# Kernel optimization log

Measured on AMD Instinct MI355X. Metric: run time of the kernel, lower is better.

## Reference

```python
import jax, jax.numpy as jnp
import numpy as np

N_EMBD = 512
N_HEADS = 8
HEAD_DIM = N_EMBD // N_HEADS
LN_EPS = 1e-5


def _layernorm(x):
    # elementwise_affine=False LayerNorm over last dim
    mu = jnp.mean(x, axis=-1, keepdims=True)
    var = jnp.mean(jnp.square(x - mu), axis=-1, keepdims=True)
    return (x - mu) * jax.lax.rsqrt(var + LN_EPS)


def setup_inputs() -> dict:
    key = jax.random.key(0)
    ks = jax.random.split(key, 9)
    B, T, C = 4, 2048, N_EMBD
    s = 0.02
    return {
        "x": jax.random.normal(ks[0], (B, T, C), jnp.float32),
        # SelfAttention: bias arg receives 0.2 (truthy) -> kqv & projection have bias
        "w_kqv": jax.random.normal(ks[1], (3 * C, C), jnp.float32) * s,
        "b_kqv": jax.random.normal(ks[2], (3 * C,), jnp.float32) * s,
        "w_proj": jax.random.normal(ks[3], (C, C), jnp.float32) * s,
        "b_proj": jax.random.normal(ks[4], (C,), jnp.float32) * s,
        # MLP: c_fc has bias=True, c_proj has bias=False
        "w_fc": jax.random.normal(ks[5], (2 * C, C), jnp.float32) * s,
        "b_fc": jax.random.normal(ks[6], (2 * C,), jnp.float32) * s,
        "w_cproj": jax.random.normal(ks[7], (C, 2 * C), jnp.float32) * s,
    }


def _attention(x, w_kqv, b_kqv, w_proj, b_proj):
    B, T, C = x.shape
    kqv = x @ w_kqv.T + b_kqv                      # (B,T,3C)
    kqv = kqv.reshape(B, T, 3, N_HEADS, HEAD_DIM)
    kqv = jnp.transpose(kqv, (2, 0, 3, 1, 4))      # (3,B,H,T,d)
    k, q, v = kqv[0], kqv[1], kqv[2]               # note: k first, as in source
    scores = jnp.einsum("bhqd,bhkd->bhqk", q, k) * (HEAD_DIM ** -0.5)
    attn = jax.nn.softmax(scores, axis=-1)         # dropout = identity (eval)
    agg = jnp.einsum("bhqk,bhkd->bhqd", attn, v)   # (B,H,T,d)
    agg = jnp.transpose(agg, (0, 2, 1, 3)).reshape(B, T, C)
    return agg @ w_proj.T + b_proj


def _mlp(x, w_fc, b_fc, w_cproj):
    h = jax.nn.gelu(x @ w_fc.T + b_fc, approximate=False)  # exact GELU (nn.GELU default)
    return h @ w_cproj.T                                   # c_proj bias=False


def reference(x, w_kqv, b_kqv, w_proj, b_proj, w_fc, b_fc, w_cproj):
    x = x + _attention(_layernorm(x), w_kqv, b_kqv, w_proj, b_proj)
    x = x + _mlp(_layernorm(x), w_fc, b_fc, w_cproj)
    return x
```

## Files before the change

kernel.cpp:

```cpp
#include <hip/hip_runtime.h>
#include <hip/hip_bf16.h>
#include <cmath>


using u16 = unsigned short;
typedef __attribute__((ext_vector_type(4))) float f32x4;
typedef __attribute__((ext_vector_type(16))) float f32x16;
typedef __attribute__((ext_vector_type(8))) short bf16x8;

constexpr int B_ = 4, T_ = 2048, C_ = 512, H_ = 8, D_ = 64;
constexpr int BT = B_ * T_;
constexpr int KQV_SEC = B_ * H_ * T_ * D_;

__device__ __forceinline__ float b2f(u16 u) {
    return __uint_as_float(((unsigned)u) << 16);
}
__device__ __forceinline__ u16 f2b(float f) {
    __hip_bfloat16 h = __float2bfloat16(f);
    return *reinterpret_cast<u16*>(&h);
}
__device__ __forceinline__ float fexp2(float x) {
    float r;
    asm("v_exp_f32 %0, %1" : "=v"(r) : "v"(x));
    return r;
}
__device__ __forceinline__ float frcp(float x) {
    float r;
    asm("v_rcp_f32 %0, %1" : "=v"(r) : "v"(x));
    return r;
}
__device__ __forceinline__ float gelu_f(float v) {
    const float ax = fabsf(v) * 0.70710678118654752f;
    const float t = frcp(1.0f + 0.3275911f * ax);
    const float y = t * (0.254829592f + t * (-0.284496736f + t * (1.421413741f +
                    t * (-1.453152027f + t * 1.061405429f))));
    const float e = fexp2(-ax * ax * 1.44269504088896f);
    float erfv = 1.0f - y * e;
    erfv = copysignf(erfv, v);
    return 0.5f * v * (1.0f + erfv);
}

__device__ __forceinline__ void gl_lds16(const u16* g, u16* l) {
    __builtin_amdgcn_global_load_lds(
        (const __attribute__((address_space(1))) unsigned int*)(const void*)g,
        (__attribute__((address_space(3))) unsigned int*)(void*)l, 16, 0, 0);
}

__device__ __forceinline__ void ln_row(const float* __restrict__ x,
                                       u16* __restrict__ o, int r, int lane) {
    const float4 a = *(const float4*)(x + (size_t)r * C_ + lane * 4);
    const float4 b = *(const float4*)(x + (size_t)r * C_ + 256 + lane * 4);
    float s = (a.x + a.y) + (a.z + a.w) + (b.x + b.y) + (b.z + b.w);
    float q = (a.x * a.x + a.y * a.y) + (a.z * a.z + a.w * a.w) +
              (b.x * b.x + b.y * b.y) + (b.z * b.z + b.w * b.w);
#pragma unroll
    for (int off = 1; off < 64; off <<= 1) {
        s += __shfl_xor(s, off, 64);
        q += __shfl_xor(q, off, 64);
    }
    const float m = s * (1.0f / C_);
    const float var = q * (1.0f / C_) - m * m;
    const float rstd = rsqrtf(var + 1e-5f);
    ushort4 u0, u1;
    u0.x = f2b((a.x - m) * rstd); u0.y = f2b((a.y - m) * rstd);
    u0.z = f2b((a.z - m) * rstd); u0.w = f2b((a.w - m) * rstd);
    u1.x = f2b((b.x - m) * rstd); u1.y = f2b((b.y - m) * rstd);
    u1.z = f2b((b.z - m) * rstd); u1.w = f2b((b.w - m) * rstd);
    *(ushort4*)(o + (size_t)r * C_ + lane * 4) = u0;
    *(ushort4*)(o + (size_t)r * C_ + 256 + lane * 4) = u1;
}

__global__ __launch_bounds__(256) void prep_k(const float* __restrict__ x,
                                              u16* __restrict__ lnout,
                                              const float* __restrict__ w0,
                                              const float* __restrict__ w1,
                                              const float* __restrict__ w2,
                                              const float* __restrict__ w3,
                                              u16* __restrict__ o0,
                                              u16* __restrict__ o1,
                                              u16* __restrict__ o2,
                                              u16* __restrict__ o3) {
    const int bid = blockIdx.x;
    const int t = threadIdx.x;
    if (bid < BT / 4) {
        ln_row(x, lnout, bid * 4 + (t >> 6), t & 63);
    } else {
        const int i = (bid - BT / 4) * 256 + t;
        const float* w; u16* o; int j;
        if (i < 196608) { w = w0; o = o0; j = i; }
        else if (i < 262144) { w = w1; o = o1; j = i - 196608; }
        else if (i < 393216) { w = w2; o = o2; j = i - 262144; }
        else { w = w3; o = o3; j = i - 393216; }
        float4 v = ((const float4*)w)[j];
        ushort4 u;
        u.x = f2b(v.x); u.y = f2b(v.y); u.z = f2b(v.z); u.w = f2b(v.w);
        ((ushort4*)o)[j] = u;
    }
}

__global__ __launch_bounds__(256) void ln_wave_k(const float* __restrict__ x,
                                                 u16* __restrict__ o) {
    ln_row(x, o, blockIdx.x * 4 + (threadIdx.x >> 6), threadIdx.x & 63);
}

template <int EPI, int MT>
__global__ __launch_bounds__(512) void gemm_mfma(const u16* __restrict__ A,
                                                 const u16* __restrict__ W,
                                                 const float* __restrict__ bias,
                                                 const float* __restrict__ resid,
                                                 void* __restrict__ out,
                                                 int K, int N) {
    __shared__ alignas(16) u16 Al[2][MT * 64];
    __shared__ alignas(16) u16 Bl[2][128 * 64];
    const int tid = threadIdx.x, lane = tid & 63, w = tid >> 6;
    const int g = lane >> 4, c = lane & 15;
    const int wm = w >> 1, wn = w & 1;
    const int n0 = blockIdx.x * 128, r0 = blockIdx.y * MT;

    const int l7 = lane & 7, l3 = lane >> 3;
    const int colHalf = ((l7 ^ l3) << 3);

    constexpr int MF = MT / 64;
    f32x4 acc[MF][4] = {};

    auto stage = [&](int buf, int kk) {
        if constexpr (MT == 128) {
#pragma unroll
            for (int i = 0; i < 2; ++i) {
                const int s = w * 2 + i;
                const int row = s * 8 + l3;
                gl_lds16(A + (size_t)(r0 + row) * K + kk + colHalf, &Al[buf][s * 512]);
            }
        } else {
            const int s = w;
            const int row = s * 8 + l3;
            gl_lds16(A + (size_t)(r0 + row) * K + kk + colHalf, &Al[buf][s * 512]);
        }
#pragma unroll
        for (int i = 0; i < 2; ++i) {
            const int s = w * 2 + i;
            const int row = s * 8 + l3;
            gl_lds16(W + (size_t)(n0 + row) * K + kk + colHalf, &Bl[buf][s * 512]);
        }
    };

    stage(0, 0);
    __syncthreads();
    const int NK = K >> 6;
    for (int k8 = 0; k8 < NK; ++k8) {
        const int buf = k8 & 1;
        if (k8 + 1 < NK) stage(buf ^ 1, (k8 + 1) * 64);
        const char* AlB = (const char*)Al[buf];
        const char* BlB = (const char*)Bl[buf];

        bf16x8 af[MF][2], bf[4][2];
#pragma unroll
        for (int mf = 0; mf < MF; ++mf) {
            const int ar = wm * (MT / 4) + mf * 16 + c;
#pragma unroll
            for (int ch = 0; ch < 2; ++ch)
                af[mf][ch] = *(const bf16x8*)(
                    AlB + ar * 128 + (((ch * 32 + g * 8) * 2) ^ ((ar & 7) << 4)));
        }
#pragma unroll
        for (int nf = 0; nf < 4; ++nf) {
            const int br = wn * 64 + nf * 16 + c;
#pragma unroll
            for (int ch = 0; ch < 2; ++ch)
                bf[nf][ch] = *(const bf16x8*)(
                    BlB + br * 128 + (((ch * 32 + g * 8) * 2) ^ ((br & 7) << 4)));
        }
#pragma unroll
        for (int mf = 0; mf < MF; ++mf)
#pragma unroll
            for (int nf = 0; nf < 4; ++nf)
#pragma unroll
                for (int ch = 0; ch < 2; ++ch)
                    acc[mf][nf] = __builtin_amdgcn_mfma_f32_16x16x32_bf16(
                        af[mf][ch], bf[nf][ch], acc[mf][nf], 0, 0, 0);
        __syncthreads();
    }

#pragma unroll
    for (int mf = 0; mf < MF; ++mf) {
#pragma unroll
        for (int nf = 0; nf < 4; ++nf) {
            const int nn = n0 + wn * 64 + nf * 16 + c;
            const int rb = r0 + wm * (MT / 4) + mf * 16 + g * 4;
            if constexpr (EPI == 0) {
                const int s = nn >> 9, rem = nn & 511;
                const int hh = rem >> 6, dd = rem & 63;
                const int bb = rb >> 11, t0 = rb & 2047;
                float v[4];
#pragma unroll
                for (int r = 0; r < 4; ++r) v[r] = acc[mf][nf][r] + bias[nn];
                if (s == 2) {
                    ushort4 u;
                    u.x = f2b(v[0]); u.y = f2b(v[1]); u.z = f2b(v[2]); u.w = f2b(v[3]);
                    *(ushort4*)((u16*)out + (size_t)2 * KQV_SEC +
                                (((size_t)(bb * H_ + hh) * D_ + dd) * T_ + t0)) = u;
                } else {
#pragma unroll
                    for (int r = 0; r < 4; ++r)
                        ((u16*)out)[(size_t)s * KQV_SEC +
                                    (((size_t)(bb * H_ + hh) * T_ + t0 + r) * D_ + dd)] = f2b(v[r]);
                }
            } else {
#pragma unroll
                for (int r = 0; r < 4; ++r) {
                    const int rr = rb + r;
                    float v = acc[mf][nf][r];
                    if constexpr (EPI != 3) v += bias[nn];
                    if constexpr (EPI == 1) {
                        v += resid[(size_t)rr * N + nn];
                        ((float*)out)[(size_t)rr * N + nn] = v;
                    } else if constexpr (EPI == 2) {
                        ((u16*)out)[(size_t)rr * N + nn] = f2b(gelu_f(v));
                    } else {
                        v += resid[(size_t)rr * N + nn];
                        ((float*)out)[(size_t)rr * N + nn] = v;
                    }
                }
            }
        }
    }
}

__global__ __launch_bounds__(256, 2) void attn_mfma9_k(const u16* __restrict__ Kb,
                                                       const u16* __restrict__ Qb,
                                                       const u16* __restrict__ VTb,
                                                       u16* __restrict__ agg) {
    __shared__ alignas(16) u16 Kl[2][128 * 64];
    __shared__ alignas(16) u16 Vl[2][64 * 128];

    const int tid = threadIdx.x;
    const int lane = tid & 63;
    const int w = tid >> 6;
    const int q = lane & 31;
    const int hi = lane >> 5;
    const int l7 = lane & 7, l3 = lane >> 3;
    const int colHalf = ((l7 ^ l3) << 3);
    const int l15 = lane & 15, l4 = lane >> 4;

    const int id = blockIdx.x;
    const int gg = id & 7, rr_ = id >> 3;
    const int qt = rr_ & 15;
    const int bh = gg * 4 + (rr_ >> 4);
    const int b = bh >> 3, h = bh & 7;
    const int q0 = qt * 128 + w * 32;

    const u16* Kbh = Kb + (size_t)bh * T_ * D_;
    const u16* Qbh = Qb + (size_t)bh * T_ * D_;
    const u16* VTbh = VTb + (size_t)bh * D_ * T_;

    bf16x8 qf[4];
#pragma unroll
    for (int ks = 0; ks < 4; ++ks) {
        bf16x8 v = *(const bf16x8*)(Qbh + (size_t)(q0 + q) * D_ + ks * 16 + hi * 8);
#pragma unroll
        for (int i = 0; i < 8; ++i)
            ((u16*)&qf[ks])[i] = f2b(b2f(((const u16*)&v)[i]) * 0.18033688011f);
    }
    bf16x8 ones8;
#pragma unroll
    for (int i = 0; i < 8; ++i) ((u16*)&ones8)[i] = 0x3F80;

    f32x16 accO0 = {}, accO1 = {}, accL = {};

    auto stageK = [&](int buf, int bt) {
#pragma unroll
        for (int i = 0; i < 4; ++i) {
            const int s = w * 4 + i;
            const int row = s * 8 + l3;
            gl_lds16(Kbh + (size_t)(bt * 128 + row) * D_ + colHalf,
                     &Kl[buf][s * 512]);
        }
    };
    auto stageV = [&](int buf, int bt) {
#pragma unroll
        for (int i = 0; i < 4; ++i) {
            const int s = w * 4 + i;
            const int row = s * 4 + l4;
            const int srcE = ((l15 ^ (row & 15)) << 3);
            gl_lds16(VTbh + (size_t)row * T_ + bt * 128 + srcE,
                     &Vl[buf][s * 512]);
        }
    };

    auto QKT = [&](int buf, int hh, f32x16& s0, f32x16& s1) {
        const char* KB = (const char*)Kl[buf];
        f32x16 a = {}, c = {};
        __builtin_amdgcn_s_setprio(1);
#pragma unroll
        for (int ks = 0; ks < 4; ++ks) {
            const int r0b = (hh * 64 + q) * 128;
            const int r1b = (hh * 64 + 32 + q) * 128;
            bf16x8 k0 = *(const bf16x8*)(KB + r0b + ((ks * 32 + hi * 16) ^ ((q & 7) << 4)));
            bf16x8 k1 = *(const bf16x8*)(KB + r1b + ((ks * 32 + hi * 16) ^ ((q & 7) << 4)));
            a = __builtin_amdgcn_mfma_f32_32x32x16_bf16(k0, qf[ks], a, 0, 0, 0);
            c = __builtin_amdgcn_mfma_f32_32x32x16_bf16(k1, qf[ks], c, 0, 0, 0);
        }
        __builtin_amdgcn_s_setprio(0);
        s0 = a; s1 = c;
    };

    auto SMPV = [&](f32x16& s0, f32x16& s1, int buf, int hh) {
        const char* VB = (const char*)Vl[buf];
        unsigned pk0[8], pk1[8];
#pragma unroll
        for (int j = 0; j < 8; ++j) {
            float a0 = fexp2(s0[2 * j]);
            float a1 = fexp2(s0[2 * j + 1]);
            float c0 = fexp2(s1[2 * j]);
            float c1 = fexp2(s1[2 * j + 1]);
            asm("v_cvt_pk_bf16_f32 %0, %1, %2" : "=v"(pk0[j]) : "v"(a0), "v"(a1));
            asm("v_cvt_pk_bf16_f32 %0, %1, %2" : "=v"(pk1[j]) : "v"(c0), "v"(c1));
        }
        __builtin_amdgcn_s_setprio(1);
#pragma unroll
        for (int ks = 0; ks < 4; ++ks) {
            const int s4 = (ks & 1) * 4;
            unsigned a0, a1, b0, b1;
            if (ks < 2) { a0 = pk0[s4]; a1 = pk0[s4 + 1]; b0 = pk0[s4 + 2]; b1 = pk0[s4 + 3]; }
            else        { a0 = pk1[s4]; a1 = pk1[s4 + 1]; b0 = pk1[s4 + 2]; b1 = pk1[s4 + 3]; }
            asm("v_permlane32_swap_b32 %0, %1" : "+v"(a0), "+v"(b0));
            asm("v_permlane32_swap_b32 %0, %1" : "+v"(a1), "+v"(b1));
            unsigned fw[4] = {a0, a1, b0, b1};
            bf16x8 pfr = *(bf16x8*)fw;
            const int colb = (hh * 128 + ks * 32 + hi * 16);
            bf16x8 v0 = *(const bf16x8*)(VB + q * 256 + (colb ^ ((q & 15) << 4)));
            bf16x8 v1 = *(const bf16x8*)(VB + (32 + q) * 256 + (colb ^ (((32 + q) & 15) << 4)));
            accL  = __builtin_amdgcn_mfma_f32_32x32x16_bf16(ones8, pfr, accL, 0, 0, 0);
            accO0 = __builtin_amdgcn_mfma_f32_32x32x16_bf16(v0, pfr, accO0, 0, 0, 0);
            accO1 = __builtin_amdgcn_mfma_f32_32x32x16_bf16(v1, pfr, accO1, 0, 0, 0);
        }
        __builtin_amdgcn_s_setprio(0);
    };

    stageK(0, 0);
    stageV(0, 0);
    __syncthreads();

    f32x16 sA0, sA1, sB0, sB1;
    for (int bt = 0; bt < 16; ++bt) {
        const int buf = bt & 1;
        if (bt + 1 < 16) {
            stageK(buf ^ 1, bt + 1);
            stageV(buf ^ 1, bt + 1);
        }
        QKT(buf, 0, sA0, sA1);
        QKT(buf, 1, sB0, sB1);
        SMPV(sA0, sA1, buf, 0);
        SMPV(sB0, sB1, buf, 1);
        __syncthreads();
    }

    const float inv = frcp(accL[0]);
    u16* outp = agg + ((size_t)b * T_ + q0 + q) * C_ + h * D_;
#pragma unroll
    for (int r2 = 0; r2 < 8; ++r2) {
        const int r = 2 * r2;
        const int d = (r & 3) + 8 * (r >> 2) + 4 * hi;
        ushort2 o0, o1;
        o0.x = f2b(accO0[r] * inv);
        o0.y = f2b(accO0[r + 1] * inv);
        o1.x = f2b(accO1[r] * inv);
        o1.y = f2b(accO1[r + 1] * inv);
        *(ushort2*)(outp + d) = o0;
        *(ushort2*)(outp + 32 + d) = o1;
    }
}

extern "C" void kernel_launch(void* const* d_in, const int* in_sizes, int n_in,
                              void* d_out, int out_size, void* d_ws, size_t ws_size,
                              hipStream_t stream) {
    (void)in_sizes; (void)n_in; (void)out_size; (void)ws_size;
    const float* x       = (const float*)d_in[0];
    const float* w_kqv   = (const float*)d_in[1];
    const float* b_kqv   = (const float*)d_in[2];
    const float* w_proj  = (const float*)d_in[3];
    const float* b_proj  = (const float*)d_in[4];
    const float* w_fc    = (const float*)d_in[5];
    const float* b_fc    = (const float*)d_in[6];
    const float* w_cproj = (const float*)d_in[7];

    char* ws = (char*)d_ws;
    u16* wq_b = (u16*)(ws + 0);
    u16* wp_b = (u16*)(ws + (1536 * 512) * 2);
    u16* wf_b = (u16*)(ws + (1536 * 512 + 512 * 512) * 2);
    u16* wc_b = (u16*)(ws + (1536 * 512 + 512 * 512 + 1024 * 512) * 2);
    u16* lnbuf = (u16*)(ws + (4ull << 20));
    u16* kqv  = (u16*)(ws + (12ull << 20));
    u16* hbuf = (u16*)(ws + (12ull << 20));
    u16* agg  = (u16*)(ws + (36ull << 20));
    float* x2 = (float*)(ws + (44ull << 20));

    prep_k<<<BT / 4 + 2048, 256, 0, stream>>>(
        x, lnbuf, w_kqv, w_proj, w_fc, w_cproj, wq_b, wp_b, wf_b, wc_b);

    gemm_mfma<0, 128><<<dim3(1536 / 128, BT / 128), 512, 0, stream>>>(
        lnbuf, wq_b, b_kqv, nullptr, kqv, 512, 1536);
    attn_mfma9_k<<<512, 256, 0, stream>>>(
        kqv, kqv + KQV_SEC, kqv + 2 * KQV_SEC, agg);
    gemm_mfma<1, 64><<<dim3(512 / 128, BT / 64), 512, 0, stream>>>(
        agg, wp_b, b_proj, x, x2, 512, 512);
    ln_wave_k<<<BT / 4, 256, 0, stream>>>(x2, lnbuf);
    gemm_mfma<2, 128><<<dim3(1024 / 128, BT / 128), 512, 0, stream>>>(
        lnbuf, wf_b, b_fc, nullptr, hbuf, 512, 1024);
    gemm_mfma<3, 64><<<dim3(512 / 128, BT / 64), 512, 0, stream>>>(
        hbuf, wc_b, nullptr, x2, d_out, 1024, 512);
}
```

Measured before the change: 133.2 us.

## Split attention KV range across two wave groups and software-pipeline QK/PV

The attention kernel now launches 512 threads per block, with two groups of four waves that each process half of the key/value sequence for the same 128 queries. Partial output accumulators and row sums from the second group are combined through shared memory at the end. The main loop is restructured into a staggered pipeline that overlaps the next tile's QK^T with the current tile's softmax/PV. This doubles in-flight waves to hide latency, at the cost of an LDS reduction step and more registers per block.

```diff
diff --git a/kernel.cpp b/kernel.cpp
--- a/kernel.cpp
+++ b/kernel.cpp
@@ -226,32 +226,35 @@
     }
 }
 
-__global__ __launch_bounds__(256, 2) void attn_mfma9_k(const u16* __restrict__ Kb,
-                                                       const u16* __restrict__ Qb,
-                                                       const u16* __restrict__ VTb,
-                                                       u16* __restrict__ agg) {
-    __shared__ alignas(16) u16 Kl[2][128 * 64];
-    __shared__ alignas(16) u16 Vl[2][64 * 128];
+__global__ __launch_bounds__(512, 2) void attn_mfma10_k(const u16* __restrict__ Kb,
+                                                        const u16* __restrict__ Qb,
+                                                        const u16* __restrict__ VTb,
+                                                        u16* __restrict__ agg) {
+    __shared__ alignas(16) u16 Kl[2][2][64 * 64];
+    __shared__ alignas(16) u16 Vl[2][2][64 * 64];
 
     const int tid = threadIdx.x;
     const int lane = tid & 63;
     const int w = tid >> 6;
+    const int half = w >> 2;
+    const int qw = w & 3;
+    const int ws = w & 3;
     const int q = lane & 31;
     const int hi = lane >> 5;
     const int l7 = lane & 7, l3 = lane >> 3;
     const int colHalf = ((l7 ^ l3) << 3);
-    const int l15 = lane & 15, l4 = lane >> 4;
 
     const int id = blockIdx.x;
     const int gg = id & 7, rr_ = id >> 3;
     const int qt = rr_ & 15;
     const int bh = gg * 4 + (rr_ >> 4);
     const int b = bh >> 3, h = bh & 7;
-    const int q0 = qt * 128 + w * 32;
+    const int q0 = qt * 128 + qw * 32;
 
     const u16* Kbh = Kb + (size_t)bh * T_ * D_;
     const u16* Qbh = Qb + (size_t)bh * T_ * D_;
     const u16* VTbh = VTb + (size_t)bh * D_ * T_;
+    const int jbase = half * 1024;
 
     bf16x8 qf[4];
 #pragma unroll
@@ -267,36 +270,33 @@
 
     f32x16 accO0 = {}, accO1 = {}, accL = {};
 
-    auto stageK = [&](int buf, int bt) {
-#pragma unroll
-        for (int i = 0; i < 4; ++i) {
-            const int s = w * 4 + i;
+    auto stageK = [&](int buf, int tt) {
+#pragma unroll
+        for (int i = 0; i < 2; ++i) {
+            const int s = ws * 2 + i;
             const int row = s * 8 + l3;
-            gl_lds16(Kbh + (size_t)(bt * 128 + row) * D_ + colHalf,
-                     &Kl[buf][s * 512]);
+            gl_lds16(Kbh + (size_t)(jbase + tt * 64 + row) * D_ + colHalf,
+                     &Kl[half][buf][s * 512]);
         }
     };
-    auto stageV = [&](int buf, int bt) {
-#pragma unroll
-        for (int i = 0; i < 4; ++i) {
-            const int s = w * 4 + i;
-            const int row = s * 4 + l4;
-            const int srcE = ((l15 ^ (row & 15)) << 3);
-            gl_lds16(VTbh + (size_t)row * T_ + bt * 128 + srcE,
-                     &Vl[buf][s * 512]);
+    auto stageV = [&](int buf, int tt) {
+#pragma unroll
+        for (int i = 0; i < 2; ++i) {
+            const int s = ws * 2 + i;
+            const int row = s * 8 + l3;
+            gl_lds16(VTbh + (size_t)row * T_ + jbase + tt * 64 + colHalf,
+                     &Vl[half][buf][s * 512]);
         }
     };
 
-    auto QKT = [&](int buf, int hh, f32x16& s0, f32x16& s1) {
-        const char* KB = (const char*)Kl[buf];
+    auto QKT = [&](int buf, f32x16& s0, f32x16& s1) {
+        const char* KB = (const char*)Kl[half][buf];
         f32x16 a = {}, c = {};
         __builtin_amdgcn_s_setprio(1);
 #pragma unroll
         for (int ks = 0; ks < 4; ++ks) {
-            const int r0b = (hh * 64 + q) * 128;
-            const int r1b = (hh * 64 + 32 + q) * 128;
-            bf16x8 k0 = *(const bf16x8*)(KB + r0b + ((ks * 32 + hi * 16) ^ ((q & 7) << 4)));
-            bf16x8 k1 = *(const bf16x8*)(KB + r1b + ((ks * 32 + hi * 16) ^ ((q & 7) << 4)));
+            bf16x8 k0 = *(const bf16x8*)(KB + q * 128 + ((ks * 32 + hi * 16) ^ ((q & 7) << 4)));
+            bf16x8 k1 = *(const bf16x8*)(KB + (32 + q) * 128 + ((ks * 32 + hi * 16) ^ ((q & 7) << 4)));
             a = __builtin_amdgcn_mfma_f32_32x32x16_bf16(k0, qf[ks], a, 0, 0, 0);
             c = __builtin_amdgcn_mfma_f32_32x32x16_bf16(k1, qf[ks], c, 0, 0, 0);
         }
@@ -304,8 +304,8 @@
         s0 = a; s1 = c;
     };
 
-    auto SMPV = [&](f32x16& s0, f32x16& s1, int buf, int hh) {
-        const char* VB = (const char*)Vl[buf];
+    auto SMPV = [&](f32x16& s0, f32x16& s1, int buf) {
+        const char* VB = (const char*)Vl[half][buf];
         unsigned pk0[8], pk1[8];
 #pragma unroll
         for (int j = 0; j < 8; ++j) {
@@ -327,9 +327,8 @@
             asm("v_permlane32_swap_b32 %0, %1" : "+v"(a1), "+v"(b1));
             unsigned fw[4] = {a0, a1, b0, b1};
             bf16x8 pfr = *(bf16x8*)fw;
-            const int colb = (hh * 128 + ks * 32 + hi * 16);
-            bf16x8 v0 = *(const bf16x8*)(VB + q * 256 + (colb ^ ((q & 15) << 4)));
-            bf16x8 v1 = *(const bf16x8*)(VB + (32 + q) * 256 + (colb ^ (((32 + q) & 15) << 4)));
+            bf16x8 v0 = *(const bf16x8*)(VB + q * 128 + ((ks * 32 + hi * 16) ^ ((q & 7) << 4)));
+            bf16x8 v1 = *(const bf16x8*)(VB + (32 + q) * 128 + ((ks * 32 + hi * 16) ^ ((q & 7) << 4)));
             accL  = __builtin_amdgcn_mfma_f32_32x32x16_bf16(ones8, pfr, accL, 0, 0, 0);
             accO0 = __builtin_amdgcn_mfma_f32_32x32x16_bf16(v0, pfr, accO0, 0, 0, 0);
             accO1 = __builtin_amdgcn_mfma_f32_32x32x16_bf16(v1, pfr, accO1, 0, 0, 0);
@@ -340,34 +339,52 @@
     stageK(0, 0);
     stageV(0, 0);
     __syncthreads();
-
+    stageK(1, 1);
     f32x16 sA0, sA1, sB0, sB1;
-    for (int bt = 0; bt < 16; ++bt) {
-        const int buf = bt & 1;
-        if (bt + 1 < 16) {
-            stageK(buf ^ 1, bt + 1);
-            stageV(buf ^ 1, bt + 1);
-        }
-        QKT(buf, 0, sA0, sA1);
-        QKT(buf, 1, sB0, sB1);
-        SMPV(sA0, sA1, buf, 0);
-        SMPV(sB0, sB1, buf, 1);
+    QKT(0, sA0, sA1);
+    stageV(1, 1);
+    __syncthreads();
+
+    for (int t = 0; t < 16; t += 2) {
+        if (t + 2 < 16) stageK(0, t + 2);
+        if (t + 1 < 16) QKT(1, sB0, sB1);
+        SMPV(sA0, sA1, 0);
         __syncthreads();
-    }
-
-    const float inv = frcp(accL[0]);
-    u16* outp = agg + ((size_t)b * T_ + q0 + q) * C_ + h * D_;
-#pragma unroll
-    for (int r2 = 0; r2 < 8; ++r2) {
-        const int r = 2 * r2;
-        const int d = (r & 3) + 8 * (r >> 2) + 4 * hi;
-        ushort2 o0, o1;
-        o0.x = f2b(accO0[r] * inv);
-        o0.y = f2b(accO0[r + 1] * inv);
-        o1.x = f2b(accO1[r] * inv);
-        o1.y = f2b(accO1[r + 1] * inv);
-        *(ushort2*)(outp + d) = o0;
-        *(ushort2*)(outp + 32 + d) = o1;
+        if (t + 2 < 16) stageV(0, t + 2);
+        if (t + 3 < 16) stageK(1, t + 3);
+        if (t + 2 < 16) QKT(0, sA0, sA1);
+        SMPV(sB0, sB1, 1);
+        __syncthreads();
+        if (t + 3 < 16) stageV(1, t + 3);
+    }
+
+    float* oS = (float*)&Kl[0][0][0];
+    float* lS = (float*)&Vl[0][0][0];
+    if (half == 1) {
+        float* oP = &oS[(qw * 64 + lane) * 32];
+#pragma unroll
+        for (int r = 0; r < 16; ++r) oP[r] = accO0[r];
+#pragma unroll
+        for (int r = 0; r < 16; ++r) oP[16 + r] = accO1[r];
+        lS[qw * 64 + lane] = accL[0];
+    }
+    __syncthreads();
+    if (half == 0) {
+        const float* oP = &oS[(qw * 64 + lane) * 32];
+        const float inv = frcp(accL[0] + lS[qw * 64 + lane]);
+        u16* outp = agg + ((size_t)b * T_ + q0 + q) * C_ + h * D_;
+#pragma unroll
+        for (int r2 = 0; r2 < 8; ++r2) {
+            const int r = 2 * r2;
+            const int d = (r & 3) + 8 * (r >> 2) + 4 * hi;
+            ushort2 o0, o1;
+            o0.x = f2b((accO0[r] + oP[r]) * inv);
+            o0.y = f2b((accO0[r + 1] + oP[r + 1]) * inv);
+            o1.x = f2b((accO1[r] + oP[16 + r]) * inv);
+            o1.y = f2b((accO1[r + 1] + oP[16 + r + 1]) * inv);
+            *(ushort2*)(outp + d) = o0;
+            *(ushort2*)(outp + 32 + d) = o1;
+        }
     }
 }
 
@@ -400,7 +417,7 @@
 
     gemm_mfma<0, 128><<<dim3(1536 / 128, BT / 128), 512, 0, stream>>>(
         lnbuf, wq_b, b_kqv, nullptr, kqv, 512, 1536);
-    attn_mfma9_k<<<512, 256, 0, stream>>>(
+    attn_mfma10_k<<<512, 512, 0, stream>>>(
         kqv, kqv + KQV_SEC, kqv + 2 * KQV_SEC, agg);
     gemm_mfma<1, 64><<<dim3(512 / 128, BT / 64), 512, 0, stream>>>(
         agg, wp_b, b_proj, x, x2, 512, 512);
```

Measured after the change: 137.3 us. 3.1% more time.
